# Kernel tuning notes

Hardware: AMD Instinct MI355X
Metric: run time of the kernel (lower is better)

The kernel has to match this reference:

```python
import jax, jax.numpy as jnp
import numpy as np

B, C, H, W = 16, 256, 128, 128
RED = 16
RATES = (1, 2, 4)  # 1 + 4 + 16 = 21 pooled values per channel


def setup_inputs() -> dict:
    key = jax.random.key(0)
    ks = jax.random.split(key, 7)
    r = C // RED
    x = jax.random.normal(ks[0], (B, C, H, W), dtype=jnp.float32)
    # stacked per-channel fusion Linears: weight (C, 21), bias (C,)
    Wf = jax.random.normal(ks[1], (C, 21), dtype=jnp.float32) * 0.2
    bf = jax.random.normal(ks[2], (C,), dtype=jnp.float32) * 0.05
    # SE bottleneck FC (stored as (in, out) so y = x @ W + b)
    W1 = jax.random.normal(ks[3], (C, r), dtype=jnp.float32) * (1.0 / np.sqrt(C))
    b1 = jax.random.normal(ks[4], (r,), dtype=jnp.float32) * 0.05
    W2 = jax.random.normal(ks[5], (r, C), dtype=jnp.float32) * (1.0 / np.sqrt(r))
    b2 = jax.random.normal(ks[6], (C,), dtype=jnp.float32) * 0.05
    return {"x": x, "Wf": Wf, "bf": bf, "W1": W1, "b1": b1, "W2": W2, "b2": b2}


def _multiscale_pool(x):
    # kernel = stride = (H//rate, W//rate) -> output rate x rate, flattened
    b, c, h, w = x.shape
    outs = []
    for rate in RATES:
        ph, pw = h // rate, w // rate
        pooled = x.reshape(b, c, rate, ph, rate, pw).max(axis=(3, 5))  # (b,c,rate,rate)
        outs.append(pooled.reshape(b, c, rate * rate))
    return jnp.concatenate(outs, axis=2)  # (b, c, 21)


def reference(x, Wf, bf, W1, b1, W2, b2):
    p = _multiscale_pool(x)                              # (B, C, 21)
    fused = jnp.einsum('bcp,cp->bc', p, Wf) + bf         # per-channel 21->1 linears
    h = jax.nn.relu(fused @ W1 + b1)                      # SE squeeze
    s = h @ W2 + b2                                       # SE excite (NOTE: original forward applies NO sigmoid)
    return x * s[:, :, None, None]
```

## Files before the change

kernel.cpp:

```cpp
#include <hip/hip_runtime.h>

#define BB 16
#define CC 256
#define HH 128
#define WW 128
#define RR 16
#define HWPLANE (HH * WW)
#define PLANE4  (HWPLANE / 4)

using f32x4 = __attribute__((ext_vector_type(4))) float;

__global__ __launch_bounds__(256) void pool_fuse_kernel(
    const float* __restrict__ x,
    const float* __restrict__ Wf,
    const float* __restrict__ bf,
    float* __restrict__ fused)
{
    const int bc = blockIdx.x;
    const int c  = bc & (CC - 1);
    const f32x4* xp = (const f32x4*)(x + (size_t)bc * HWPLANE);

    const int t    = threadIdx.x;
    const int lane = t & 63;
    const int wave = t >> 6;
    const int bx   = (t & 31) >> 3;

    __shared__ float wred[4][16];
    __shared__ float pb[16];

#pragma unroll
    for (int by = 0; by < 4; ++by) {
        float m = -3.402823466e+38f;
#pragma unroll
        for (int ii = 0; ii < 4; ++ii) {
            const int i = by * 4 + ii;
            f32x4 v = xp[i * 256 + t];
            m = fmaxf(m, fmaxf(fmaxf(v.x, v.y), fmaxf(v.z, v.w)));
        }
        m = fmaxf(m, __shfl_xor(m, 1));
        m = fmaxf(m, __shfl_xor(m, 2));
        m = fmaxf(m, __shfl_xor(m, 4));
        m = fmaxf(m, __shfl_xor(m, 32));
        if ((lane & 7) == 0 && lane < 32) wred[wave][by * 4 + bx] = m;
    }
    __syncthreads();

    if (t < 16) {
        pb[t] = fmaxf(fmaxf(wred[0][t], wred[1][t]),
                      fmaxf(wred[2][t], wred[3][t]));
    }
    __syncthreads();

    if (t == 0) {
        float q0 = fmaxf(fmaxf(pb[0],  pb[1]),  fmaxf(pb[4],  pb[5]));
        float q1 = fmaxf(fmaxf(pb[2],  pb[3]),  fmaxf(pb[6],  pb[7]));
        float q2 = fmaxf(fmaxf(pb[8],  pb[9]),  fmaxf(pb[12], pb[13]));
        float q3 = fmaxf(fmaxf(pb[10], pb[11]), fmaxf(pb[14], pb[15]));
        float g  = fmaxf(fmaxf(q0, q1), fmaxf(q2, q3));

        const float* w = Wf + c * 21;
        float acc = bf[c] + g * w[0]
                  + q0 * w[1] + q1 * w[2] + q2 * w[3] + q3 * w[4];
#pragma unroll
        for (int k = 0; k < 16; ++k) acc += pb[k] * w[5 + k];
        fused[bc] = acc;
    }
}

__global__ __launch_bounds__(256) void se_kernel(
    const float* __restrict__ fused,
    const float* __restrict__ W1,
    const float* __restrict__ b1,
    const float* __restrict__ W2,
    const float* __restrict__ b2,
    float* __restrict__ s)
{
    __shared__ float hl[BB][RR];
    const int t = threadIdx.x;

    {
        const int b = t >> 4, j = t & 15;
        float acc = b1[j];
        for (int cc = 0; cc < CC; ++cc)
            acc += fused[b * CC + cc] * W1[cc * RR + j];
        hl[b][j] = fmaxf(acc, 0.0f);
    }
    __syncthreads();

#pragma unroll
    for (int k = 0; k < BB; ++k) {
        float acc = b2[t];
#pragma unroll
        for (int j = 0; j < RR; ++j)
            acc += hl[k][j] * W2[j * CC + t];
        s[k * CC + t] = acc;
    }
}

__global__ __launch_bounds__(256) void scale_kernel(
    const float* __restrict__ x,
    const float* __restrict__ s,
    float* __restrict__ out)
{
    const int bc = blockIdx.x;
    const float sc = s[bc];
    const f32x4* xp = (const f32x4*)(x + (size_t)bc * HWPLANE);
    f32x4* op = (f32x4*)(out + (size_t)bc * HWPLANE);
    const int t = threadIdx.x;

#pragma unroll
    for (int i = 0; i < 16; ++i) {
        f32x4 v = xp[i * 256 + t];
        f32x4 o = v * sc;
        __builtin_nontemporal_store(o, &op[i * 256 + t]);
    }
}

extern "C" void kernel_launch(void* const* d_in, const int* in_sizes, int n_in,
                              void* d_out, int out_size, void* d_ws, size_t ws_size,
                              hipStream_t stream) {
    const float* x  = (const float*)d_in[0];
    const float* Wf = (const float*)d_in[1];
    const float* bf = (const float*)d_in[2];
    const float* W1 = (const float*)d_in[3];
    const float* b1 = (const float*)d_in[4];
    const float* W2 = (const float*)d_in[5];
    const float* b2 = (const float*)d_in[6];
    float* out = (float*)d_out;

    float* fused = (float*)d_ws;
    float* s     = fused + BB * CC;

    pool_fuse_kernel<<<BB * CC, 256, 0, stream>>>(x, Wf, bf, fused);
    se_kernel<<<1, 256, 0, stream>>>(fused, W1, b1, W2, b2, s);
    scale_kernel<<<BB * CC, 256, 0, stream>>>(x, s, out);
}
```

Measured before the change: 141.1 us.

## Fuse pool, SE and scale into one persistent kernel with grid barriers

Replaces the three kernels with a single persistent kernel of 512 blocks that processes the planes in four stages of four batches each. In each stage every block pools two planes, a software grid barrier publishes the fused values, each block recomputes the SE bottleneck for its batch, then rescales its planes. Reading x again right after pooling it is meant to hit in L2/MALL instead of DRAM, and two launches are removed. The cost is four grid-wide barriers, redundant SE math in every block, and the requirement that all 512 blocks be co-resident, otherwise the kernel deadlocks.

After: 362.9 us. 157% more time.

```diff
diff --git a/kernel.cpp b/kernel.cpp
--- a/kernel.cpp
+++ b/kernel.cpp
@@ -2,117 +2,153 @@
 
 #define BB 16
 #define CC 256
-#define HH 128
-#define WW 128
 #define RR 16
-#define HWPLANE (HH * WW)
-#define PLANE4  (HWPLANE / 4)
+#define HWPLANE 16384
+#define NBLOCKS 512
+#define NSTAGES 4
+#define PLANES_PER_STAGE 1024
+#define PPB 2
 
 using f32x4 = __attribute__((ext_vector_type(4))) float;
 
-__global__ __launch_bounds__(256) void pool_fuse_kernel(
+__global__ void init_kernel(unsigned* bar) {
+    if (threadIdx.x < 2) bar[threadIdx.x] = 0u;
+}
+
+__device__ __forceinline__ void grid_barrier(unsigned* cnt, unsigned* gen) {
+    __syncthreads();
+    if (threadIdx.x == 0) {
+        unsigned g = __hip_atomic_load(gen, __ATOMIC_RELAXED,
+                                       __HIP_MEMORY_SCOPE_AGENT);
+        unsigned arrived = __hip_atomic_fetch_add(cnt, 1u, __ATOMIC_ACQ_REL,
+                                                  __HIP_MEMORY_SCOPE_AGENT);
+        if (arrived == NBLOCKS - 1) {
+            __hip_atomic_store(cnt, 0u, __ATOMIC_RELAXED,
+                               __HIP_MEMORY_SCOPE_AGENT);
+            __hip_atomic_fetch_add(gen, 1u, __ATOMIC_RELEASE,
+                                   __HIP_MEMORY_SCOPE_AGENT);
+        } else {
+            while (__hip_atomic_load(gen, __ATOMIC_ACQUIRE,
+                                     __HIP_MEMORY_SCOPE_AGENT) == g) {
+                __builtin_amdgcn_s_sleep(8);
+            }
+        }
+    }
+    __syncthreads();
+}
+
+__global__ __launch_bounds__(256, 4) void spse_fused_kernel(
     const float* __restrict__ x,
     const float* __restrict__ Wf,
     const float* __restrict__ bf,
+    const float* __restrict__ W1,
+    const float* __restrict__ b1,
+    const float* __restrict__ W2,
+    const float* __restrict__ b2,
+    float* __restrict__ out,
+    unsigned* __restrict__ bar,
     float* __restrict__ fused)
 {
-    const int bc = blockIdx.x;
-    const int c  = bc & (CC - 1);
-    const f32x4* xp = (const f32x4*)(x + (size_t)bc * HWPLANE);
-
     const int t    = threadIdx.x;
     const int lane = t & 63;
     const int wave = t >> 6;
     const int bx   = (t & 31) >> 3;
+    const int blk  = blockIdx.x;
 
     __shared__ float wred[4][16];
-    __shared__ float pb[16];
+    __shared__ float pb[PPB][16];
+    __shared__ float hpart[16][16];
+    __shared__ float hl[RR];
+    __shared__ float sv[PPB];
 
+    for (int stage = 0; stage < NSTAGES; ++stage) {
+        const int bc0 = stage * PLANES_PER_STAGE + blk * PPB;
+
+        for (int q = 0; q < PPB; ++q) {
+            const f32x4* xp = (const f32x4*)(x + (size_t)(bc0 + q) * HWPLANE);
 #pragma unroll
-    for (int by = 0; by < 4; ++by) {
-        float m = -3.402823466e+38f;
+            for (int by = 0; by < 4; ++by) {
+                float m = -3.402823466e+38f;
 #pragma unroll
-        for (int ii = 0; ii < 4; ++ii) {
-            const int i = by * 4 + ii;
-            f32x4 v = xp[i * 256 + t];
-            m = fmaxf(m, fmaxf(fmaxf(v.x, v.y), fmaxf(v.z, v.w)));
+                for (int ii = 0; ii < 4; ++ii) {
+                    f32x4 v = xp[(by * 4 + ii) * 256 + t];
+                    m = fmaxf(m, fmaxf(fmaxf(v.x, v.y), fmaxf(v.z, v.w)));
+                }
+                m = fmaxf(m, __shfl_xor(m, 1));
+                m = fmaxf(m, __shfl_xor(m, 2));
+                m = fmaxf(m, __shfl_xor(m, 4));
+                m = fmaxf(m, __shfl_xor(m, 32));
+                if ((lane & 7) == 0 && lane < 32) wred[wave][by * 4 + bx] = m;
+            }
+            __syncthreads();
+            if (t < 16)
+                pb[q][t] = fmaxf(fmaxf(wred[0][t], wred[1][t]),
+                                 fmaxf(wred[2][t], wred[3][t]));
+            __syncthreads();
         }
-        m = fmaxf(m, __shfl_xor(m, 1));
-        m = fmaxf(m, __shfl_xor(m, 2));
-        m = fmaxf(m, __shfl_xor(m, 4));
-        m = fmaxf(m, __shfl_xor(m, 32));
-        if ((lane & 7) == 0 && lane < 32) wred[wave][by * 4 + bx] = m;
-    }
-    __syncthreads();
 
-    if (t < 16) {
-        pb[t] = fmaxf(fmaxf(wred[0][t], wred[1][t]),
-                      fmaxf(wred[2][t], wred[3][t]));
-    }
-    __syncthreads();
+        if (t < PPB) {
+            const int bc = bc0 + t;
+            const int c  = bc & (CC - 1);
+            const float* p = pb[t];
+            float q0 = fmaxf(fmaxf(p[0],  p[1]),  fmaxf(p[4],  p[5]));
+            float q1 = fmaxf(fmaxf(p[2],  p[3]),  fmaxf(p[6],  p[7]));
+            float q2 = fmaxf(fmaxf(p[8],  p[9]),  fmaxf(p[12], p[13]));
+            float q3 = fmaxf(fmaxf(p[10], p[11]), fmaxf(p[14], p[15]));
+            float gm = fmaxf(fmaxf(q0, q1), fmaxf(q2, q3));
+            const float* w = Wf + c * 21;
+            float acc = bf[c] + gm * w[0]
+                      + q0 * w[1] + q1 * w[2] + q2 * w[3] + q3 * w[4];
+#pragma unroll
+            for (int k = 0; k < 16; ++k) acc += p[k] * w[5 + k];
+            __hip_atomic_store(&fused[bc], acc, __ATOMIC_RELAXED,
+                               __HIP_MEMORY_SCOPE_AGENT);
+        }
 
-    if (t == 0) {
-        float q0 = fmaxf(fmaxf(pb[0],  pb[1]),  fmaxf(pb[4],  pb[5]));
-        float q1 = fmaxf(fmaxf(pb[2],  pb[3]),  fmaxf(pb[6],  pb[7]));
-        float q2 = fmaxf(fmaxf(pb[8],  pb[9]),  fmaxf(pb[12], pb[13]));
-        float q3 = fmaxf(fmaxf(pb[10], pb[11]), fmaxf(pb[14], pb[15]));
-        float g  = fmaxf(fmaxf(q0, q1), fmaxf(q2, q3));
+        grid_barrier(&bar[0], &bar[1]);
 
-        const float* w = Wf + c * 21;
-        float acc = bf[c] + g * w[0]
-                  + q0 * w[1] + q1 * w[2] + q2 * w[3] + q3 * w[4];
+        const int b = bc0 >> 8;
+        {
+            const int j = t & 15, ch = t >> 4;
+            float p = 0.f;
 #pragma unroll
-        for (int k = 0; k < 16; ++k) acc += pb[k] * w[5 + k];
-        fused[bc] = acc;
-    }
-}
+            for (int m = 0; m < 16; ++m) {
+                const int cc = ch * 16 + m;
+                float fv = __hip_atomic_load(&fused[b * CC + cc],
+                                             __ATOMIC_RELAXED,
+                                             __HIP_MEMORY_SCOPE_AGENT);
+                p += fv * W1[cc * RR + j];
+            }
+            hpart[ch][j] = p;
+        }
+        __syncthreads();
+        if (t < RR) {
+            float a = b1[t];
+#pragma unroll
+            for (int ch = 0; ch < 16; ++ch) a += hpart[ch][t];
+            hl[t] = fmaxf(a, 0.f);
+        }
+        __syncthreads();
+        if (t < PPB) {
+            const int c = (bc0 + t) & (CC - 1);
+            float a = b2[c];
+#pragma unroll
+            for (int j = 0; j < RR; ++j) a += hl[j] * W2[j * CC + c];
+            sv[t] = a;
+        }
+        __syncthreads();
 
-__global__ __launch_bounds__(256) void se_kernel(
-    const float* __restrict__ fused,
-    const float* __restrict__ W1,
-    const float* __restrict__ b1,
-    const float* __restrict__ W2,
-    const float* __restrict__ b2,
-    float* __restrict__ s)
-{
-    __shared__ float hl[BB][RR];
-    const int t = threadIdx.x;
-
-    {
-        const int b = t >> 4, j = t & 15;
-        float acc = b1[j];
-        for (int cc = 0; cc < CC; ++cc)
-            acc += fused[b * CC + cc] * W1[cc * RR + j];
-        hl[b][j] = fmaxf(acc, 0.0f);
-    }
-    __syncthreads();
-
+        for (int q = 0; q < PPB; ++q) {
+            const float sc = sv[q];
+            const f32x4* xp = (const f32x4*)(x + (size_t)(bc0 + q) * HWPLANE);
+            f32x4* op = (f32x4*)(out + (size_t)(bc0 + q) * HWPLANE);
 #pragma unroll
-    for (int k = 0; k < BB; ++k) {
-        float acc = b2[t];
-#pragma unroll
-        for (int j = 0; j < RR; ++j)
-            acc += hl[k][j] * W2[j * CC + t];
-        s[k * CC + t] = acc;
-    }
-}
-
-__global__ __launch_bounds__(256) void scale_kernel(
-    const float* __restrict__ x,
-    const float* __restrict__ s,
-    float* __restrict__ out)
-{
-    const int bc = blockIdx.x;
-    const float sc = s[bc];
-    const f32x4* xp = (const f32x4*)(x + (size_t)bc * HWPLANE);
-    f32x4* op = (f32x4*)(out + (size_t)bc * HWPLANE);
-    const int t = threadIdx.x;
-
-#pragma unroll
-    for (int i = 0; i < 16; ++i) {
-        f32x4 v = xp[i * 256 + t];
-        f32x4 o = v * sc;
-        __builtin_nontemporal_store(o, &op[i * 256 + t]);
+            for (int i = 0; i < 16; ++i) {
+                f32x4 v = xp[i * 256 + t];
+                __builtin_nontemporal_store(v * sc, &op[i * 256 + t]);
+            }
+        }
+        __syncthreads();
     }
 }
 
@@ -128,10 +164,10 @@
     const float* b2 = (const float*)d_in[6];
     float* out = (float*)d_out;
 
-    float* fused = (float*)d_ws;
-    float* s     = fused + BB * CC;
+    unsigned* bar  = (unsigned*)d_ws;
+    float* fused   = (float*)((char*)d_ws + 256);
 
-    pool_fuse_kernel<<<BB * CC, 256, 0, stream>>>(x, Wf, bf, fused);
-    se_kernel<<<1, 256, 0, stream>>>(fused, W1, b1, W2, b2, s);
-    scale_kernel<<<BB * CC, 256, 0, stream>>>(x, s, out);
+    init_kernel<<<1, 64, 0, stream>>>(bar);
+    spse_fused_kernel<<<NBLOCKS, 256, 0, stream>>>(
+        x, Wf, bf, W1, b1, W2, b2, out, bar, fused);
 }
```

## Split pool/scale into batch groups for LLC reuse and fuse SE into scale

Applied to the files above, without the earlier changes.

The work is now processed in four groups of 1024 planes. Each group runs the pooling kernel and then the scale kernel, so the second read of x can hit the large last-level cache instead of going back to HBM. The single-block SE kernel is removed. Each scale block recomputes its batch's squeeze/excite from the fused values, which drops one serialized launch. The cost is more kernel launches, more tail effects between groups, and a small amount of redundant SE arithmetic in every block.

Measured after the change: 137.6 us. 2.5% less time.

```diff
diff --git a/kernel.cpp b/kernel.cpp
--- a/kernel.cpp
+++ b/kernel.cpp
@@ -2,11 +2,10 @@
 
 #define BB 16
 #define CC 256
-#define HH 128
-#define WW 128
 #define RR 16
-#define HWPLANE (HH * WW)
-#define PLANE4  (HWPLANE / 4)
+#define HWPLANE 16384
+#define NGROUPS 4
+#define PLANES_PER_GROUP 1024
 
 using f32x4 = __attribute__((ext_vector_type(4))) float;
 
@@ -14,9 +13,10 @@
     const float* __restrict__ x,
     const float* __restrict__ Wf,
     const float* __restrict__ bf,
-    float* __restrict__ fused)
+    float* __restrict__ fused,
+    int plane0)
 {
-    const int bc = blockIdx.x;
+    const int bc = plane0 + blockIdx.x;
     const int c  = bc & (CC - 1);
     const f32x4* xp = (const f32x4*)(x + (size_t)bc * HWPLANE);
 
@@ -33,8 +33,7 @@
         float m = -3.402823466e+38f;
 #pragma unroll
         for (int ii = 0; ii < 4; ++ii) {
-            const int i = by * 4 + ii;
-            f32x4 v = xp[i * 256 + t];
+            f32x4 v = xp[(by * 4 + ii) * 256 + t];
             m = fmaxf(m, fmaxf(fmaxf(v.x, v.y), fmaxf(v.z, v.w)));
         }
         m = fmaxf(m, __shfl_xor(m, 1));
@@ -45,10 +44,9 @@
     }
     __syncthreads();
 
-    if (t < 16) {
+    if (t < 16)
         pb[t] = fmaxf(fmaxf(wred[0][t], wred[1][t]),
                       fmaxf(wred[2][t], wred[3][t]));
-    }
     __syncthreads();
 
     if (t == 0) {
@@ -67,52 +65,58 @@
     }
 }
 
-__global__ __launch_bounds__(256) void se_kernel(
-    const float* __restrict__ fused,
+__global__ __launch_bounds__(256) void scale_se_kernel(
+    const float* __restrict__ x,
     const float* __restrict__ W1,
     const float* __restrict__ b1,
     const float* __restrict__ W2,
     const float* __restrict__ b2,
-    float* __restrict__ s)
+    const float* __restrict__ fused,
+    float* __restrict__ out,
+    int plane0)
 {
-    __shared__ float hl[BB][RR];
-    const int t = threadIdx.x;
+    const int bc = plane0 + blockIdx.x;
+    const int b  = bc >> 8;
+    const int c  = bc & (CC - 1);
+    const int t  = threadIdx.x;
+
+    __shared__ float hpart[16][16];
+    __shared__ float hl[RR];
+    __shared__ float svs;
 
     {
-        const int b = t >> 4, j = t & 15;
-        float acc = b1[j];
-        for (int cc = 0; cc < CC; ++cc)
-            acc += fused[b * CC + cc] * W1[cc * RR + j];
-        hl[b][j] = fmaxf(acc, 0.0f);
+        const int j = t & 15, ch = t >> 4;
+        float p = 0.f;
+#pragma unroll
+        for (int m = 0; m < 16; ++m) {
+            const int cc = ch * 16 + m;
+            p += fused[b * CC + cc] * W1[cc * RR + j];
+        }
+        hpart[ch][j] = p;
+    }
+    __syncthreads();
+    if (t < RR) {
+        float a = b1[t];
+#pragma unroll
+        for (int ch = 0; ch < 16; ++ch) a += hpart[ch][t];
+        hl[t] = fmaxf(a, 0.f);
+    }
+    __syncthreads();
+    if (t == 0) {
+        float a = b2[c];
+#pragma unroll
+        for (int j = 0; j < RR; ++j) a += hl[j] * W2[j * CC + c];
+        svs = a;
     }
     __syncthreads();
 
-#pragma unroll
-    for (int k = 0; k < BB; ++k) {
-        float acc = b2[t];
-#pragma unroll
-        for (int j = 0; j < RR; ++j)
-            acc += hl[k][j] * W2[j * CC + t];
-        s[k * CC + t] = acc;
-    }
-}
-
-__global__ __launch_bounds__(256) void scale_kernel(
-    const float* __restrict__ x,
-    const float* __restrict__ s,
-    float* __restrict__ out)
-{
-    const int bc = blockIdx.x;
-    const float sc = s[bc];
+    const float sc = svs;
     const f32x4* xp = (const f32x4*)(x + (size_t)bc * HWPLANE);
     f32x4* op = (f32x4*)(out + (size_t)bc * HWPLANE);
-    const int t = threadIdx.x;
-
 #pragma unroll
     for (int i = 0; i < 16; ++i) {
         f32x4 v = xp[i * 256 + t];
-        f32x4 o = v * sc;
-        __builtin_nontemporal_store(o, &op[i * 256 + t]);
+        __builtin_nontemporal_store(v * sc, &op[i * 256 + t]);
     }
 }
 
@@ -129,9 +133,12 @@
     float* out = (float*)d_out;
 
     float* fused = (float*)d_ws;
-    float* s     = fused + BB * CC;
 
-    pool_fuse_kernel<<<BB * CC, 256, 0, stream>>>(x, Wf, bf, fused);
-    se_kernel<<<1, 256, 0, stream>>>(fused, W1, b1, W2, b2, s);
-    scale_kernel<<<BB * CC, 256, 0, stream>>>(x, s, out);
+    for (int g = 0; g < NGROUPS; ++g) {
+        const int plane0 = g * PLANES_PER_GROUP;
+        pool_fuse_kernel<<<PLANES_PER_GROUP, 256, 0, stream>>>(
+            x, Wf, bf, fused, plane0);
+        scale_se_kernel<<<PLANES_PER_GROUP, 256, 0, stream>>>(
+            x, W1, b1, W2, b2, fused, out, plane0);
+    }
 }
```
